# Kernel tuning notes

Measured on AMD Instinct MI355X. Metric: run time of the kernel, lower is better.

## Reference

```python
import jax, jax.numpy as jnp
import numpy as np

HIDDEN = 1024
N_HEAD = 16
HEAD_DIM = HIDDEN // N_HEAD  # 64
BATCH = 1
SEQ = 4096
THETA = 10000.0


def _rope_cos_sin(seq_len, head_dim, dtype=jnp.float32):
    # freqs[t, j] = t / theta^(2j/dim), j in [0, dim/2)
    inv_freq = 1.0 / (THETA ** (jnp.arange(0, head_dim, 2, dtype=dtype) / head_dim))
    t = jnp.arange(seq_len, dtype=dtype)
    freqs = jnp.outer(t, inv_freq)           # [S, D/2]
    return jnp.cos(freqs), jnp.sin(freqs)


def _apply_rope(x, cos, sin):
    # x: [B, S, H, D]; pairs (x[...,2j], x[...,2j+1]) rotated by angle freqs[t, j]
    x2 = x.reshape(*x.shape[:-1], -1, 2)       # [B, S, H, D/2, 2]
    x_re, x_im = x2[..., 0], x2[..., 1]
    c = cos[None, :, None, :]                   # [1, S, 1, D/2]
    s = sin[None, :, None, :]
    out_re = x_re * c - x_im * s
    out_im = x_re * s + x_im * c
    out = jnp.stack([out_re, out_im], axis=-1)  # [B, S, H, D/2, 2]
    return out.reshape(x.shape)


def setup_inputs() -> dict:
    key = jax.random.key(0)
    kx, kq, kk, kv = jax.random.split(key, 4)
    scale = 1.0 / np.sqrt(HIDDEN)
    return {
        "x": jax.random.normal(kx, (BATCH, SEQ, HIDDEN), dtype=jnp.float32),
        "wq": jax.random.normal(kq, (HIDDEN, HIDDEN), dtype=jnp.float32) * scale,
        "wk": jax.random.normal(kk, (HIDDEN, HIDDEN), dtype=jnp.float32) * scale,
        "wv": jax.random.normal(kv, (HIDDEN, HIDDEN), dtype=jnp.float32) * scale,
    }


def reference(x, wq, wk, wv):
    B, S, _ = x.shape
    # torch nn.Linear(no bias): y = x @ W.T
    xq = (x @ wq.T).reshape(B, S, N_HEAD, HEAD_DIM).astype(jnp.float32)
    xk = (x @ wk.T).reshape(B, S, N_HEAD, HEAD_DIM).astype(jnp.float32)
    xv = (x @ wv.T).reshape(B, S, N_HEAD, HEAD_DIM).astype(jnp.float32)

    cos, sin = _rope_cos_sin(S, HEAD_DIM)
    q = _apply_rope(xq, cos, sin)
    k = _apply_rope(xk, cos, sin)

    # [B, H, S, S] scores, no causal mask (matches source)
    scores = jnp.einsum("bqhd,bkhd->bhqk", q, k) / jnp.sqrt(
        jnp.asarray(HEAD_DIM, dtype=q.dtype))
    attn = jax.nn.softmax(scores, axis=-1)
    out = jnp.einsum("bhqk,bkhd->bqhd", attn, xv)  # [B, S, H, D]
    return out.reshape(B, S, N_HEAD * HEAD_DIM)
```

## Files before the change

### kernel.cpp

```cpp
#include <hip/hip_runtime.h>
#include <stdint.h>


#define SEQLEN 4096
#define NHEAD 16
#define HDIM 64

typedef __bf16 bf16x8 __attribute__((ext_vector_type(8)));
typedef float f32x4 __attribute__((ext_vector_type(4)));
typedef float f32x16 __attribute__((ext_vector_type(16)));

__device__ __forceinline__ unsigned short f2bf(float f) {
  union { float f; unsigned int u; } v; v.f = f;
  unsigned int r = v.u + 0x7FFFu + ((v.u >> 16) & 1u);
  return (unsigned short)(r >> 16);
}
__device__ __forceinline__ unsigned int pkc(float lo, float hi) {
  union { __bf16 b[2]; unsigned int u; } z;
  z.b[0] = (__bf16)lo; z.b[1] = (__bf16)hi;
  return z.u;
}
__device__ __forceinline__ bf16x8 as_bf(uint4 v) { return __builtin_bit_cast(bf16x8, v); }
__device__ __forceinline__ f32x4 mfma16(bf16x8 a, bf16x8 b, f32x4 c) {
  return __builtin_amdgcn_mfma_f32_16x16x32_bf16(a, b, c, 0, 0, 0);
}
__device__ __forceinline__ f32x16 mfma32(bf16x8 a, bf16x8 b, f32x16 c) {
  return __builtin_amdgcn_mfma_f32_32x32x16_bf16(a, b, c, 0, 0, 0);
}
__device__ __forceinline__ void gll16(const void* g, void* l) {
  __builtin_amdgcn_global_load_lds(
      (const __attribute__((address_space(1))) void*)g,
      (__attribute__((address_space(3))) void*)l, 16, 0, 0);
}

__global__ __launch_bounds__(256) void k_convert(
    const float* __restrict__ x, const float* __restrict__ wq,
    const float* __restrict__ wk, const float* __restrict__ wv,
    unsigned short* __restrict__ xbf, unsigned short* __restrict__ wbf) {
  int i = blockIdx.x * 256 + threadIdx.x;
  const int NX = SEQLEN * 1024 / 4;
  const int NW = 1024 * 1024 / 4;
  float4 v;
  unsigned short* dst;
  int di;
  if (i < NX) {
    v = ((const float4*)x)[i]; dst = xbf; di = i;
  } else {
    int j = i - NX;
    const float4* src = (const float4*)((j < NW) ? wq : (j < 2 * NW) ? wk : wv);
    v = src[j & (NW - 1)];
    dst = wbf; di = j;
  }
  ushort4 o; o.x = f2bf(v.x); o.y = f2bf(v.y); o.z = f2bf(v.z); o.w = f2bf(v.w);
  ((ushort4*)dst)[di] = o;
}

__global__ __launch_bounds__(256) void k_table(float* __restrict__ ct, float* __restrict__ st) {
  int i = blockIdx.x * 256 + threadIdx.x;
  int s = i >> 5, j = i & 31;
  double inv = exp(-(double)j * 0.28782313662425572);
  double a = (double)s * inv;
  ct[i] = (float)cos(a);
  st[i] = (float)sin(a);
}

__global__ __launch_bounds__(256) void k_gemm(
    const unsigned short* __restrict__ xbf, const unsigned short* __restrict__ wbf,
    const float* __restrict__ ct, const float* __restrict__ st,
    unsigned short* __restrict__ qbf, unsigned short* __restrict__ KF,
    unsigned short* __restrict__ VF) {
  __shared__ __align__(16) unsigned short As[2][128 * 32];
  __shared__ __align__(16) unsigned short Bs[2][128 * 32];
  const int t = threadIdx.x;
  const int bn = blockIdx.x, bm = blockIdx.y;
  const int lane = t & 63, wave = t >> 6;
  const int r = lane & 15, g = lane >> 4;
  const int wm = wave >> 1, wn = wave & 1;

  const int c0 = 2 * wave, c1 = 2 * wave + 1;
  const int srowA = lane >> 2, sb = (lane & 3) * 16;
  const char* gA0 = (const char*)xbf + (size_t)(bm * 128 + 16 * c0 + srowA) * 2048 + sb;
  const char* gA1 = (const char*)xbf + (size_t)(bm * 128 + 16 * c1 + srowA) * 2048 + sb;
  const char* gB0 = (const char*)wbf + (size_t)(bn * 128 + 16 * c0 + srowA) * 2048 + sb;
  const char* gB1 = (const char*)wbf + (size_t)(bn * 128 + 16 * c1 + srowA) * 2048 + sb;

  gll16(gA0, (char*)As[0] + c0 * 1024);
  gll16(gA1, (char*)As[0] + c1 * 1024);
  gll16(gB0, (char*)Bs[0] + c0 * 1024);
  gll16(gB1, (char*)Bs[0] + c1 * 1024);
  gA0 += 64; gA1 += 64; gB0 += 64; gB1 += 64;

  f32x4 zero4 = {0.f, 0.f, 0.f, 0.f};
  f32x4 acc[4][4];
#pragma unroll
  for (int m = 0; m < 4; ++m)
#pragma unroll
    for (int n = 0; n < 4; ++n) acc[m][n] = zero4;

  for (int kk = 0; kk < 32; ++kk) {
    __syncthreads();
    if (kk < 31) {
      char* Ad = (char*)As[(kk + 1) & 1];
      char* Bd = (char*)Bs[(kk + 1) & 1];
      gll16(gA0, Ad + c0 * 1024);
      gll16(gA1, Ad + c1 * 1024);
      gll16(gB0, Bd + c0 * 1024);
      gll16(gB1, Bd + c1 * 1024);
      gA0 += 64; gA1 += 64; gB0 += 64; gB1 += 64;
    }
    const char* Ac = (const char*)As[kk & 1];
    const char* Bc = (const char*)Bs[kk & 1];
    bf16x8 af[4], bfr[4];
#pragma unroll
    for (int m = 0; m < 4; ++m)
      af[m] = as_bf(*(const uint4*)(Ac + (wm * 64 + m * 16 + r) * 64 + g * 16));
#pragma unroll
    for (int n = 0; n < 4; ++n)
      bfr[n] = as_bf(*(const uint4*)(Bc + (wn * 64 + n * 16 + r) * 64 + g * 16));
#pragma unroll
    for (int m = 0; m < 4; ++m)
#pragma unroll
      for (int n = 0; n < 4; ++n)
        acc[m][n] = mfma16(af[m], bfr[n], acc[m][n]);
  }

  const int matid = bn >> 3;
#pragma unroll
  for (int m = 0; m < 4; ++m) {
    const int row0 = bm * 128 + wm * 64 + m * 16 + 4 * g;
#pragma unroll
    for (int n = 0; n < 4; ++n) {
      const int col = bn * 128 + wn * 64 + n * 16 + r;
      const int d = col & 63;
      const int hh = (col >> 6) & 15;
      if (matid < 2) {
        const int jdx = (col >> 1) & 31;
        const float sgn = (col & 1) ? 1.0f : -1.0f;
        const float qs = (matid == 0) ? 0.18033688011112042f : 1.0f;
        size_t kfi0 = (size_t)hh * 262144 + (size_t)(row0 >> 5) * 2048 +
                      (size_t)((d >> 4) & 3) * 512 +
                      (size_t)((((d >> 3) & 1) * 32) + (row0 & 31)) * 8 + (d & 7);
#pragma unroll
        for (int j = 0; j < 4; ++j) {
          float v = acc[m][n][j];
          float p = __shfl_xor(v, 1);
          int srow = row0 + j;
          float cv = ct[srow * 32 + jdx];
          float sv = st[srow * 32 + jdx];
          float o = (v * cv + p * sv * sgn) * qs;
          if (matid == 0) {
            qbf[(size_t)srow * 1024 + (hh * 64 + d)] = f2bf(o);
          } else {
            KF[kfi0 + (size_t)j * 8] = f2bf(o);
          }
        }
      } else {
        ushort4 o;
        o.x = f2bf(acc[m][n][0]); o.y = f2bf(acc[m][n][1]);
        o.z = f2bf(acc[m][n][2]); o.w = f2bf(acc[m][n][3]);
        const int kt = row0 >> 5, q4 = (row0 >> 2) & 7;
        const int kc = q4 >> 2, bb = (q4 >> 1) & 1, h2 = q4 & 1;
        const int dt = d >> 5, l2 = d & 31;
        size_t off = (size_t)hh * 524288 + (size_t)kt * 4096 + (size_t)dt * 2048 +
                     (size_t)kc * 1024 + (size_t)(h2 * 32 + l2) * 16 + bb * 8;
        *(ushort4*)((char*)VF + off) = o;
      }
    }
  }
}

__global__ __launch_bounds__(512) void k_attn(
    const unsigned short* __restrict__ qbf, const unsigned short* __restrict__ KF,
    const unsigned short* __restrict__ VF, float* __restrict__ out) {
  __shared__ __align__(16) char smem[33280];
  const int t = threadIdx.x;
  const int b = blockIdx.x;
  const int work = (b & 7) * 64 + (b >> 3);
  const int h = work >> 5;
  const int qb = work & 31;
  const int lane = t & 63, wave = t >> 6;
  const int qw = wave & 3, hf = wave >> 2;
  const int li = lane & 31, hi = lane >> 5;
  const int q0 = qb * 128 + qw * 32;

  bf16x8 qf[4];
#pragma unroll
  for (int c = 0; c < 4; ++c)
    qf[c] = as_bf(*(const uint4*)((const char*)qbf +
              (size_t)(q0 + li) * 2048 + h * 128 + c * 32 + hi * 16));

  f32x16 z16 = {0.f};
  f32x16 acc[2];
  acc[0] = z16; acc[1] = z16;
  float l4[4] = {0.f, 0.f, 0.f, 0.f};

  const char* pK = (const char*)KF + (size_t)h * 524288 + (size_t)hf * 262144 + lane * 16;
  const char* pV = (const char*)VF + (size_t)h * 524288 + (size_t)hf * 262144 + lane * 16;

  const int start = wave * 8;

  for (int jj = 0; jj < 64; ++jj) {
    const int j = (start + jj) & 63;
    const char* tK = pK + ((size_t)j << 12);
    const char* tV = pV + ((size_t)j << 12);
    bf16x8 kf[4];
#pragma unroll
    for (int c = 0; c < 4; ++c)
      kf[c] = as_bf(*(const uint4*)(tK + c * 1024));
    bf16x8 vf2[2][2];
#pragma unroll
    for (int dt = 0; dt < 2; ++dt)
#pragma unroll
      for (int kc = 0; kc < 2; ++kc)
        vf2[dt][kc] = as_bf(*(const uint4*)(tV + dt * 2048 + kc * 1024));

    f32x16 sT = z16;
    __builtin_amdgcn_s_setprio(1);
#pragma unroll
    for (int c = 0; c < 4; ++c)
      sT = mfma32(kf[c], qf[c], sT);
    __builtin_amdgcn_s_setprio(0);

#pragma unroll
    for (int i = 0; i < 16; ++i) sT[i] = __builtin_amdgcn_exp2f(sT[i]);

#pragma unroll
    for (int i = 0; i < 4; ++i)
      l4[i] += (sT[i] + sT[i + 4]) + (sT[i + 8] + sT[i + 12]);

    bf16x8 pfr[2];
#pragma unroll
    for (int kc = 0; kc < 2; ++kc) {
      const int bix = kc * 8;
      uint4 bw;
      bw.x = pkc(sT[bix + 0], sT[bix + 1]);
      bw.y = pkc(sT[bix + 2], sT[bix + 3]);
      bw.z = pkc(sT[bix + 4], sT[bix + 5]);
      bw.w = pkc(sT[bix + 6], sT[bix + 7]);
      pfr[kc] = as_bf(bw);
    }
    __builtin_amdgcn_s_setprio(1);
#pragma unroll
    for (int kc = 0; kc < 2; ++kc) {
      acc[0] = mfma32(vf2[0][kc], pfr[kc], acc[0]);
      acc[1] = mfma32(vf2[1][kc], pfr[kc], acc[1]);
    }
    __builtin_amdgcn_s_setprio(0);
  }

  float lrun = (l4[0] + l4[1]) + (l4[2] + l4[3]);
  float lhalf = lrun + __shfl_xor(lrun, 32);

  __syncthreads();
  float* shm = (float*)smem;
  if (hf == 1) {
    float* ab = shm + qw * 2048;
#pragma unroll
    for (int dt = 0; dt < 2; ++dt)
#pragma unroll
      for (int i = 0; i < 16; ++i) {
        int d = (i & 3) + 8 * (i >> 2) + 4 * hi + 32 * dt;
        ab[d * 32 + li] = acc[dt][i];
      }
    if (hi == 0) shm[8192 + qw * 32 + li] = lhalf;
  }
  __syncthreads();
  if (hf == 0) {
    float* ab = shm + qw * 2048;
    float l1 = shm[8192 + qw * 32 + li];
    float linv = 1.0f / (lhalf + l1);
#pragma unroll
    for (int dt = 0; dt < 2; ++dt)
#pragma unroll
      for (int i = 0; i < 16; ++i) {
        int d = (i & 3) + 8 * (i >> 2) + 4 * hi + 32 * dt;
        acc[dt][i] = (acc[dt][i] + ab[d * 32 + li]) * linv;
      }
    __asm__ volatile("" ::: "memory");

    float* eb = shm + qw * 2048;
#pragma unroll
    for (int dt = 0; dt < 2; ++dt) {
#pragma unroll
      for (int i = 0; i < 16; ++i)
        eb[li * 33 + ((i & 3) + 8 * (i >> 2) + 4 * hi)] = acc[dt][i];
      __asm__ volatile("" ::: "memory");
#pragma unroll
      for (int it = 0; it < 16; ++it) {
        int q = it * 2 + hi;
        float v = eb[q * 33 + li];
        out[(size_t)(q0 + q) * 1024 + h * 64 + dt * 32 + li] = v;
      }
      __asm__ volatile("" ::: "memory");
    }
  }
}

extern "C" void kernel_launch(void* const* d_in, const int* in_sizes, int n_in,
                              void* d_out, int out_size, void* d_ws, size_t ws_size,
                              hipStream_t stream) {
  const float* x  = (const float*)d_in[0];
  const float* wq = (const float*)d_in[1];
  const float* wk = (const float*)d_in[2];
  const float* wv = (const float*)d_in[3];
  float* out = (float*)d_out;
  char* ws = (char*)d_ws;

  unsigned short* qbf = (unsigned short*)(ws);
  unsigned short* KF  = (unsigned short*)(ws + ((size_t)8 << 20));
  unsigned short* VF  = (unsigned short*)(ws + ((size_t)16 << 20));
  unsigned short* xbf = (unsigned short*)(ws + ((size_t)24 << 20));
  unsigned short* wbf = (unsigned short*)(ws + ((size_t)32 << 20));
  float* ct = (float*)(ws + ((size_t)38 << 20));
  float* st = (float*)(ws + ((size_t)38 << 20) + ((size_t)512 << 10));

  k_convert<<<dim3(7168), dim3(256), 0, stream>>>(x, wq, wk, wv, xbf, wbf);
  k_table<<<dim3(512), dim3(256), 0, stream>>>(ct, st);
  k_gemm<<<dim3(24, 32), dim3(256), 0, stream>>>(xbf, wbf, ct, st, qbf, KF, VF);
  k_attn<<<dim3(512), dim3(512), 0, stream>>>(qbf, KF, VF, out);
}
```

Measured before the change: 161.2 us.

## Merge prep kernels, interleave RoPE table, stage K epilogue through LDS

Merges the bf16 conversion and RoPE table kernels into one launch and stores cos/sin interleaved as float2 so each lookup is a single load. The K projection epilogue now writes rotated values into swizzled LDS and then emits coalesced 16-byte stores in the attention-friendly KF layout, replacing scattered 2-byte global stores. This adds extra LDS traffic and barriers to the K-producing blocks only.

```diff
diff --git a/kernel.cpp b/kernel.cpp
--- a/kernel.cpp
+++ b/kernel.cpp
@@ -33,44 +33,44 @@
       (__attribute__((address_space(3))) void*)l, 16, 0, 0);
 }
 
-__global__ __launch_bounds__(256) void k_convert(
+__global__ __launch_bounds__(256) void k_prep(
     const float* __restrict__ x, const float* __restrict__ wq,
     const float* __restrict__ wk, const float* __restrict__ wv,
-    unsigned short* __restrict__ xbf, unsigned short* __restrict__ wbf) {
-  int i = blockIdx.x * 256 + threadIdx.x;
+    unsigned short* __restrict__ xbf, unsigned short* __restrict__ wbf,
+    float2* __restrict__ ctst) {
   const int NX = SEQLEN * 1024 / 4;
   const int NW = 1024 * 1024 / 4;
-  float4 v;
-  unsigned short* dst;
-  int di;
-  if (i < NX) {
-    v = ((const float4*)x)[i]; dst = xbf; di = i;
+  if (blockIdx.x < 7168) {
+    int i = blockIdx.x * 256 + threadIdx.x;
+    float4 v;
+    unsigned short* dst;
+    int di;
+    if (i < NX) {
+      v = ((const float4*)x)[i]; dst = xbf; di = i;
+    } else {
+      int j = i - NX;
+      const float4* src = (const float4*)((j < NW) ? wq : (j < 2 * NW) ? wk : wv);
+      v = src[j & (NW - 1)];
+      dst = wbf; di = j;
+    }
+    ushort4 o; o.x = f2bf(v.x); o.y = f2bf(v.y); o.z = f2bf(v.z); o.w = f2bf(v.w);
+    ((ushort4*)dst)[di] = o;
   } else {
-    int j = i - NX;
-    const float4* src = (const float4*)((j < NW) ? wq : (j < 2 * NW) ? wk : wv);
-    v = src[j & (NW - 1)];
-    dst = wbf; di = j;
-  }
-  ushort4 o; o.x = f2bf(v.x); o.y = f2bf(v.y); o.z = f2bf(v.z); o.w = f2bf(v.w);
-  ((ushort4*)dst)[di] = o;
-}
-
-__global__ __launch_bounds__(256) void k_table(float* __restrict__ ct, float* __restrict__ st) {
-  int i = blockIdx.x * 256 + threadIdx.x;
-  int s = i >> 5, j = i & 31;
-  double inv = exp(-(double)j * 0.28782313662425572);
-  double a = (double)s * inv;
-  ct[i] = (float)cos(a);
-  st[i] = (float)sin(a);
+    int i = (blockIdx.x - 7168) * 256 + threadIdx.x;
+    int s = i >> 5, j = i & 31;
+    double inv = exp(-(double)j * 0.28782313662425572);
+    double a = (double)s * inv;
+    float2 cs; cs.x = (float)cos(a); cs.y = (float)sin(a);
+    ctst[i] = cs;
+  }
 }
 
 __global__ __launch_bounds__(256) void k_gemm(
     const unsigned short* __restrict__ xbf, const unsigned short* __restrict__ wbf,
-    const float* __restrict__ ct, const float* __restrict__ st,
+    const float2* __restrict__ ctst,
     unsigned short* __restrict__ qbf, unsigned short* __restrict__ KF,
     unsigned short* __restrict__ VF) {
-  __shared__ __align__(16) unsigned short As[2][128 * 32];
-  __shared__ __align__(16) unsigned short Bs[2][128 * 32];
+  __shared__ __align__(16) char lds[32768];
   const int t = threadIdx.x;
   const int bn = blockIdx.x, bm = blockIdx.y;
   const int lane = t & 63, wave = t >> 6;
@@ -84,10 +84,10 @@
   const char* gB0 = (const char*)wbf + (size_t)(bn * 128 + 16 * c0 + srowA) * 2048 + sb;
   const char* gB1 = (const char*)wbf + (size_t)(bn * 128 + 16 * c1 + srowA) * 2048 + sb;
 
-  gll16(gA0, (char*)As[0] + c0 * 1024);
-  gll16(gA1, (char*)As[0] + c1 * 1024);
-  gll16(gB0, (char*)Bs[0] + c0 * 1024);
-  gll16(gB1, (char*)Bs[0] + c1 * 1024);
+  gll16(gA0, lds + c0 * 1024);
+  gll16(gA1, lds + c1 * 1024);
+  gll16(gB0, lds + 16384 + c0 * 1024);
+  gll16(gB1, lds + 16384 + c1 * 1024);
   gA0 += 64; gA1 += 64; gB0 += 64; gB1 += 64;
 
   f32x4 zero4 = {0.f, 0.f, 0.f, 0.f};
@@ -100,16 +100,16 @@
   for (int kk = 0; kk < 32; ++kk) {
     __syncthreads();
     if (kk < 31) {
-      char* Ad = (char*)As[(kk + 1) & 1];
-      char* Bd = (char*)Bs[(kk + 1) & 1];
+      char* Ad = lds + ((kk + 1) & 1) * 8192;
+      char* Bd = lds + 16384 + ((kk + 1) & 1) * 8192;
       gll16(gA0, Ad + c0 * 1024);
       gll16(gA1, Ad + c1 * 1024);
       gll16(gB0, Bd + c0 * 1024);
       gll16(gB1, Bd + c1 * 1024);
       gA0 += 64; gA1 += 64; gB0 += 64; gB1 += 64;
     }
-    const char* Ac = (const char*)As[kk & 1];
-    const char* Bc = (const char*)Bs[kk & 1];
+    const char* Ac = lds + (kk & 1) * 8192;
+    const char* Bc = lds + 16384 + (kk & 1) * 8192;
     bf16x8 af[4], bfr[4];
 #pragma unroll
     for (int m = 0; m < 4; ++m)
@@ -125,45 +125,73 @@
   }
 
   const int matid = bn >> 3;
-#pragma unroll
-  for (int m = 0; m < 4; ++m) {
-    const int row0 = bm * 128 + wm * 64 + m * 16 + 4 * g;
-#pragma unroll
-    for (int n = 0; n < 4; ++n) {
-      const int col = bn * 128 + wn * 64 + n * 16 + r;
-      const int d = col & 63;
-      const int hh = (col >> 6) & 15;
-      if (matid < 2) {
-        const int jdx = (col >> 1) & 31;
-        const float sgn = (col & 1) ? 1.0f : -1.0f;
-        const float qs = (matid == 0) ? 0.18033688011112042f : 1.0f;
-        size_t kfi0 = (size_t)hh * 262144 + (size_t)(row0 >> 5) * 2048 +
-                      (size_t)((d >> 4) & 3) * 512 +
-                      (size_t)((((d >> 3) & 1) * 32) + (row0 & 31)) * 8 + (d & 7);
+  if (matid == 1) {
+    __syncthreads();
+#pragma unroll
+    for (int m = 0; m < 4; ++m) {
+      const int rl0 = wm * 64 + m * 16 + 4 * g;
+#pragma unroll
+      for (int n = 0; n < 4; ++n) {
+        const int cl = wn * 64 + n * 16 + r;
+        const int jdx = (cl >> 1) & 31;
+        const float sgn = (cl & 1) ? 1.0f : -1.0f;
 #pragma unroll
         for (int j = 0; j < 4; ++j) {
           float v = acc[m][n][j];
           float p = __shfl_xor(v, 1);
-          int srow = row0 + j;
-          float cv = ct[srow * 32 + jdx];
-          float sv = st[srow * 32 + jdx];
-          float o = (v * cv + p * sv * sgn) * qs;
-          if (matid == 0) {
+          const int rl = rl0 + j;
+          float2 cs = ctst[(bm * 128 + rl) * 32 + jdx];
+          float o = v * cs.x + p * cs.y * sgn;
+          const int byte = rl * 256 + ((2 * cl) ^ ((rl & 15) << 4));
+          *(unsigned short*)(lds + byte) = f2bf(o);
+        }
+      }
+    }
+    __syncthreads();
+#pragma unroll
+    for (int it = 0; it < 8; ++it) {
+      const int e = it * 256 + t;
+      const int h2 = e >> 10, ktl = (e >> 8) & 3, c = (e >> 6) & 3, ln = e & 63;
+      const int row = ktl * 32 + (ln & 31);
+      const int col = h2 * 64 + c * 16 + (ln >> 5) * 8;
+      uint4 v = *(const uint4*)(lds + row * 256 + ((2 * col) ^ ((row & 15) << 4)));
+      size_t off = (size_t)((bn - 8) * 2 + h2) * 524288 +
+                   (size_t)(bm * 4 + ktl) * 4096 + (size_t)c * 1024 + (size_t)ln * 16;
+      *(uint4*)((char*)KF + off) = v;
+    }
+  } else {
+#pragma unroll
+    for (int m = 0; m < 4; ++m) {
+      const int row0 = bm * 128 + wm * 64 + m * 16 + 4 * g;
+#pragma unroll
+      for (int n = 0; n < 4; ++n) {
+        const int col = bn * 128 + wn * 64 + n * 16 + r;
+        const int d = col & 63;
+        const int hh = (col >> 6) & 15;
+        if (matid == 0) {
+          const int jdx = (col >> 1) & 31;
+          const float sgn = (col & 1) ? 1.0f : -1.0f;
+          const float qs = 0.18033688011112042f;
+#pragma unroll
+          for (int j = 0; j < 4; ++j) {
+            float v = acc[m][n][j];
+            float p = __shfl_xor(v, 1);
+            int srow = row0 + j;
+            float2 cs = ctst[srow * 32 + jdx];
+            float o = (v * cs.x + p * cs.y * sgn) * qs;
             qbf[(size_t)srow * 1024 + (hh * 64 + d)] = f2bf(o);
-          } else {
-            KF[kfi0 + (size_t)j * 8] = f2bf(o);
           }
+        } else {
+          ushort4 o;
+          o.x = f2bf(acc[m][n][0]); o.y = f2bf(acc[m][n][1]);
+          o.z = f2bf(acc[m][n][2]); o.w = f2bf(acc[m][n][3]);
+          const int kt = row0 >> 5, q4 = (row0 >> 2) & 7;
+          const int kc = q4 >> 2, bb = (q4 >> 1) & 1, h2v = q4 & 1;
+          const int dt = d >> 5, l2 = d & 31;
+          size_t off = (size_t)hh * 524288 + (size_t)kt * 4096 + (size_t)dt * 2048 +
+                       (size_t)kc * 1024 + (size_t)(h2v * 32 + l2) * 16 + bb * 8;
+          *(ushort4*)((char*)VF + off) = o;
         }
-      } else {
-        ushort4 o;
-        o.x = f2bf(acc[m][n][0]); o.y = f2bf(acc[m][n][1]);
-        o.z = f2bf(acc[m][n][2]); o.w = f2bf(acc[m][n][3]);
-        const int kt = row0 >> 5, q4 = (row0 >> 2) & 7;
-        const int kc = q4 >> 2, bb = (q4 >> 1) & 1, h2 = q4 & 1;
-        const int dt = d >> 5, l2 = d & 31;
-        size_t off = (size_t)hh * 524288 + (size_t)kt * 4096 + (size_t)dt * 2048 +
-                     (size_t)kc * 1024 + (size_t)(h2 * 32 + l2) * 16 + bb * 8;
-        *(ushort4*)((char*)VF + off) = o;
       }
     }
   }
@@ -311,11 +339,9 @@
   unsigned short* VF  = (unsigned short*)(ws + ((size_t)16 << 20));
   unsigned short* xbf = (unsigned short*)(ws + ((size_t)24 << 20));
   unsigned short* wbf = (unsigned short*)(ws + ((size_t)32 << 20));
-  float* ct = (float*)(ws + ((size_t)38 << 20));
-  float* st = (float*)(ws + ((size_t)38 << 20) + ((size_t)512 << 10));
-
-  k_convert<<<dim3(7168), dim3(256), 0, stream>>>(x, wq, wk, wv, xbf, wbf);
-  k_table<<<dim3(512), dim3(256), 0, stream>>>(ct, st);
-  k_gemm<<<dim3(24, 32), dim3(256), 0, stream>>>(xbf, wbf, ct, st, qbf, KF, VF);
+  float2* ctst = (float2*)(ws + ((size_t)38 << 20));
+
+  k_prep<<<dim3(7680), dim3(256), 0, stream>>>(x, wq, wk, wv, xbf, wbf, ctst);
+  k_gemm<<<dim3(24, 32), dim3(256), 0, stream>>>(xbf, wbf, ctst, qbf, KF, VF);
   k_attn<<<dim3(512), dim3(512), 0, stream>>>(qbf, KF, VF, out);
 }
```

Result: slower. 164.5 us (+2.0%).
